# Kernel optimization log

Hardware: AMD Instinct MI355X
Metric: run time of the kernel (lower is better)

## Reference

```python
import jax, jax.numpy as jnp
import numpy as np

M = 64; N_SC = 32; SPS = 8; LENCP = 16; NUMOFDM = 256 // N_SC
BETA = 0.5; SPAN = 16; LENRRC = SPAN * SPS + 1  # 129
FC = 25e6; FS = 10e6 * SPS
CLIP = 1.2; SNR = 10.0; THRES = 8.0
LEN_T = NUMOFDM * (M + LENCP)              # 640
NUMSAMPLES = LEN_T * SPS + LENRRC * 2      # 5378
L1 = LEN_T * SPS + LENRRC - 1              # 5248 (post pulse-shaping length)


def make_rrc():
    # standard root-raised-cosine, unit energy
    t = np.arange(-SPAN * SPS // 2, SPAN * SPS // 2 + 1) / SPS
    h = np.zeros_like(t)
    eps = 1e-9
    t0 = np.abs(t) < eps
    ts = np.abs(np.abs(t) - 1.0 / (4 * BETA)) < eps
    reg = ~(t0 | ts)
    tr = t[reg]
    h[reg] = (np.sin(np.pi * tr * (1 - BETA)) + 4 * BETA * tr * np.cos(np.pi * tr * (1 + BETA))) / (
        np.pi * tr * (1 - (4 * BETA * tr) ** 2))
    h[t0] = 1 + BETA * (4 / np.pi - 1)
    h[ts] = (BETA / np.sqrt(2)) * ((1 + 2 / np.pi) * np.sin(np.pi / (4 * BETA)) +
                                   (1 - 2 / np.pi) * np.cos(np.pi / (4 * BETA)))
    h = h / np.sqrt(np.sum(h ** 2))
    return h.astype(np.float32)


def _conv_full(u, k):
    # torch F.conv1d(x, k.flip(), padding=K-1) == full convolution with k
    K = k.shape[0]
    return jax.lax.conv_general_dilated(
        u[:, None, :], k[::-1][None, None, :], (1,), [(K - 1, K - 1)],
        dimension_numbers=('NCH', 'OIH', 'NCH'))[:, 0, :]


def _pulse_filter(c, rrc):
    return _conv_full(c.real, rrc) + 1j * _conv_full(c.imag, rrc)


def _power_norm(z):
    m = jnp.mean(z, axis=1, keepdims=True)
    s = jnp.std(z, axis=1, ddof=1, keepdims=True)  # torch.std is unbiased
    return (z - m) / (s + 1e-8)


def _forward(x, W_enc, b_enc, W_dec, b_dec, rrc, awgn, startloc):
    B = x.shape[0]
    # --- encoder (linear proxy for ResNetTx) -> 512 reals ---
    z = x.reshape(B, -1) @ W_enc + b_enc
    z = _power_norm(z)
    c = z.reshape(B, 256, 2)
    c = (c[..., 0] + 1j * c[..., 1]).reshape(B, NUMOFDM, N_SC)  # complex64
    # --- DFT precoding ---
    c = jnp.fft.fftshift(jnp.fft.fft(c, axis=-1, norm='ortho'), axes=-1)
    # --- subcarrier mapping (contiguous block, mapping==1) ---
    loc = jnp.arange(startloc, startloc + N_SC)
    data_f = jnp.zeros((B, NUMOFDM, M), jnp.complex64).at[:, :, loc].set(c)
    data_t = jnp.fft.ifft(data_f, axis=-1, norm='ortho')
    data_t = jnp.concatenate([data_t[:, :, -LENCP:], data_t], axis=-1)  # CP
    data_t = data_t.reshape(B, LEN_T)
    # --- zero-stuffed upsampling + RRC pulse shaping ---
    over = jnp.zeros((B, LEN_T * SPS), jnp.complex64).at[:, ::SPS].set(data_t)
    xc = _pulse_filter(over, rrc)  # (B, L1)
    # --- carrier mixing ---
    n = jnp.arange(NUMSAMPLES, dtype=jnp.float32)
    cos_c = jnp.sqrt(2.0) * jnp.cos(2 * jnp.pi * FC * n / FS)
    sin_c = jnp.sqrt(2.0) * jnp.sin(2 * jnp.pi * FC * n / FS)
    data_x = xc.real * cos_c[:L1] - xc.imag * sin_c[:L1]
    # --- clipping ---
    thr = CLIP * jnp.sqrt(jnp.mean(jnp.square(data_x), axis=1, keepdims=True))
    over_amp = jax.nn.relu(jnp.abs(data_x) - thr)
    data_x = (1.0 - over_amp / (jnp.abs(data_x) + 1e-8)) * data_x
    # --- PAPR ---
    tstart = (LENRRC + 1) // 2
    p = jnp.square(data_x[:, tstart:tstart + LEN_T * SPS])
    PAPRdB = 10.0 * jnp.log10(jnp.max(p, axis=1) / jnp.mean(p, axis=1))
    PAPRloss = jnp.mean(jax.nn.relu(PAPRdB - THRES))
    # --- AWGN channel (no fading) ---
    data_r = data_x + awgn
    # --- downconversion + matched filter ---
    rc = data_r * cos_c[:L1] - 1j * (data_r * sin_c[:L1])
    filt = _pulse_filter(rc, rrc)  # (B, L1 + LENRRC - 1) = (B, 5376)
    y = filt[:, LENRRC - 1:filt.shape[1] - LENRRC:SPS]  # (B, LEN_T)
    y = y.reshape(B, NUMOFDM, M + LENCP)[:, :, LENCP:]
    y = jnp.fft.fft(y, axis=-1, norm='ortho')[:, :, loc]
    y = jnp.fft.ifft(jnp.fft.fftshift(y, axes=-1), axis=-1, norm='ortho')
    y = y.reshape(B, NUMOFDM * N_SC)
    y = jnp.stack([y.real, y.imag], axis=-1).reshape(B, 8, 8, 8)
    # --- decoder (linear proxy for ResNetRx) ---
    out = (y.reshape(B, 512) @ W_dec + b_dec).reshape(B, 3, 32, 32)
    return out, PAPRdB, PAPRloss


def setup_inputs() -> dict:
    key = jax.random.key(0)
    ks = jax.random.split(key, 4)
    B = 1024
    x = jax.random.normal(ks[0], (B, 3, 32, 32), jnp.float32)
    W_enc = jax.random.normal(ks[1], (3072, 512), jnp.float32) * 0.02
    b_enc = jnp.zeros((512,), jnp.float32)
    W_dec = jax.random.normal(ks[2], (512, 3072), jnp.float32) * 0.05
    b_dec = jnp.zeros((3072,), jnp.float32)
    rrc = jnp.asarray(make_rrc())
    noise_std = 10.0 ** (-SNR / 20.0)
    awgn = jax.random.normal(ks[3], (B, L1), jnp.float32) * noise_std
    return {"x": x, "W_enc": W_enc, "b_enc": b_enc, "W_dec": W_dec,
            "b_dec": b_dec, "rrc": rrc, "awgn": awgn, "startloc": 7}


def reference(x, W_enc, b_enc, W_dec, b_dec, rrc, awgn, startloc):
    return _forward(x, W_enc, b_enc, W_dec, b_dec, rrc, awgn, startloc)
```

## Files before the change

### kernel.cpp

```cpp
#include <hip/hip_runtime.h>
#include <hip/hip_bf16.h>
#include <math.h>

#define L1_     5248
#define LENRRC_ 129
#define TSTART_ 65
#define NWIN_   5120
#define SWZ(m) ((m) + ((m) >> 3))

typedef __attribute__((ext_vector_type(8))) short s16x8;
typedef __attribute__((ext_vector_type(4))) float f32x4;

__device__ inline ushort bf16_rne(float x) {
    unsigned xb = __float_as_uint(x);
    return (ushort)((xb + 0x7fffu + ((xb >> 16) & 1u)) >> 16);
}

__device__ inline float wave_sum(float v) {
    #pragma unroll
    for (int m = 32; m > 0; m >>= 1) v += __shfl_xor(v, m, 64);
    return v;
}
__device__ inline float wave_max(float v) {
    #pragma unroll
    for (int m = 32; m > 0; m >>= 1) v = fmaxf(v, __shfl_xor(v, m, 64));
    return v;
}

__global__ __launch_bounds__(256) void pack_k(const float* __restrict__ x,
        const float* __restrict__ W1, const float* __restrict__ W2,
        const float* __restrict__ benc,
        ushort* __restrict__ xb, ushort* __restrict__ w1t, ushort* __restrict__ w2t,
        float* __restrict__ z)
{
    __shared__ ushort tile[64][70];
    const int blk = blockIdx.x, tid = threadIdx.x;
    if (blk < 3072) {
        int i = blk * 256 + tid;
        float4 v = ((const float4*)x)[i];
        ushort4 h;
        h.x = bf16_rne(v.x); h.y = bf16_rne(v.y);
        h.z = bf16_rne(v.z); h.w = bf16_rne(v.w);
        ((ushort4*)xb)[i] = h;
    } else if (blk < 3840) {
        const float* W; ushort* T; int K, N, n0, k0;
        if (blk < 3456) {
            int idx = blk - 3072;
            W = W1; T = w1t; K = 3072; N = 512;
            n0 = (idx & 7) * 64; k0 = (idx >> 3) * 64;
        } else {
            int idx = blk - 3456;
            W = W2; T = w2t; K = 512; N = 3072;
            n0 = (idx % 48) * 64; k0 = (idx / 48) * 64;
        }
        const int cr = tid >> 4, cc = (tid & 15) * 4;
        #pragma unroll
        for (int i = 0; i < 4; ++i) {
            int kk = i * 16 + cr;
            float4 v = *(const float4*)&W[(size_t)(k0 + kk) * N + n0 + cc];
            tile[kk][cc]     = bf16_rne(v.x);
            tile[kk][cc + 1] = bf16_rne(v.y);
            tile[kk][cc + 2] = bf16_rne(v.z);
            tile[kk][cc + 3] = bf16_rne(v.w);
        }
        __syncthreads();
        #pragma unroll
        for (int i = 0; i < 4; ++i) {
            int nn = i * 16 + cr;
            ushort4 h;
            h.x = tile[cc][nn]; h.y = tile[cc + 1][nn];
            h.z = tile[cc + 2][nn]; h.w = tile[cc + 3][nn];
            *(ushort4*)&T[(size_t)(n0 + nn) * K + k0 + cc] = h;
        }
    } else {
        int i = (blk - 3840) * 256 + tid;
        z[i] = benc[i & 511];
    }
}

__global__ __launch_bounds__(256) void gemm1_k(const ushort* __restrict__ Ab,
        const ushort* __restrict__ Bb, float* __restrict__ C, int M, int N, int K,
        int partial)
{
    __shared__ ushort Asl[64 * 72];
    __shared__ ushort Bsl[128 * 72];
    const int tid = threadIdx.x;
    const int lane = tid & 63, wave = tid >> 6;
    const int wm = (wave >> 1) * 32, wn = (wave & 1) * 64;
    const int m0 = blockIdx.y * 64, n0 = blockIdx.x * 128;
    const int kch = K / 8, kbeg = blockIdx.z * kch, kend = kbeg + kch;
    const int fm = lane & 15, q = lane >> 4;
    f32x4 acc[2][4] = {};

    for (int kt = kbeg; kt < kend; kt += 64) {
        #pragma unroll
        for (int i = 0; i < 2; ++i) {
            int c = i * 256 + tid;
            int row = c >> 3, k8 = (c & 7) * 8;
            *(uint4*)&Asl[row * 72 + k8] =
                *(const uint4*)&Ab[(size_t)(m0 + row) * K + kt + k8];
        }
        #pragma unroll
        for (int i = 0; i < 4; ++i) {
            int c = i * 256 + tid;
            int row = c >> 3, k8 = (c & 7) * 8;
            *(uint4*)&Bsl[row * 72 + k8] =
                *(const uint4*)&Bb[(size_t)(n0 + row) * K + kt + k8];
        }
        __syncthreads();
        #pragma unroll
        for (int ks = 0; ks < 2; ++ks) {
            s16x8 a[2], b[4];
            #pragma unroll
            for (int mf = 0; mf < 2; ++mf)
                a[mf] = *(const s16x8*)&Asl[(wm + mf * 16 + fm) * 72 + ks * 32 + q * 8];
            #pragma unroll
            for (int nf = 0; nf < 4; ++nf)
                b[nf] = *(const s16x8*)&Bsl[(wn + nf * 16 + fm) * 72 + ks * 32 + q * 8];
            #pragma unroll
            for (int mf = 0; mf < 2; ++mf)
                #pragma unroll
                for (int nf = 0; nf < 4; ++nf)
                    acc[mf][nf] = __builtin_amdgcn_mfma_f32_16x16x32_bf16(a[mf], b[nf], acc[mf][nf], 0, 0, 0);
        }
        __syncthreads();
    }

    if (partial) {
        float* Cs = C + (size_t)blockIdx.z * ((size_t)M * N);
        #pragma unroll
        for (int mf = 0; mf < 2; ++mf)
            #pragma unroll
            for (int nf = 0; nf < 4; ++nf)
                #pragma unroll
                for (int r = 0; r < 4; ++r) {
                    int m = m0 + wm + mf * 16 + q * 4 + r;
                    int n = n0 + wn + nf * 16 + fm;
                    Cs[(size_t)m * N + n] = acc[mf][nf][r];
                }
    } else {
        #pragma unroll
        for (int mf = 0; mf < 2; ++mf)
            #pragma unroll
            for (int nf = 0; nf < 4; ++nf)
                #pragma unroll
                for (int r = 0; r < 4; ++r) {
                    int m = m0 + wm + mf * 16 + q * 4 + r;
                    int n = n0 + wn + nf * 16 + fm;
                    atomicAdd(&C[(size_t)m * N + n], acc[mf][nf][r]);
                }
    }
}

__global__ __launch_bounds__(256) void gemm2_k(const ushort* __restrict__ Ab,
        const ushort* __restrict__ Bb, const float* __restrict__ bias,
        const float* __restrict__ papr, float* __restrict__ C,
        float* __restrict__ out_loss, int M, int N, int K)
{
    __shared__ ushort Asl[64 * 72];
    __shared__ ushort Bsl[64 * 72];
    __shared__ float red[4];
    const int tid = threadIdx.x;
    const int lane = tid & 63, wave = tid >> 6;
    const int wm = (wave >> 1) * 32, wn = (wave & 1) * 32;
    const int m0 = blockIdx.y * 64, n0 = blockIdx.x * 64;
    const int fm = lane & 15, q = lane >> 4;
    f32x4 acc[2][2] = {};

    for (int kt = 0; kt < K; kt += 64) {
        #pragma unroll
        for (int i = 0; i < 2; ++i) {
            int c = i * 256 + tid;
            int row = c >> 3, k8 = (c & 7) * 8;
            *(uint4*)&Asl[row * 72 + k8] =
                *(const uint4*)&Ab[(size_t)(m0 + row) * K + kt + k8];
            *(uint4*)&Bsl[row * 72 + k8] =
                *(const uint4*)&Bb[(size_t)(n0 + row) * K + kt + k8];
        }
        __syncthreads();
        #pragma unroll
        for (int ks = 0; ks < 2; ++ks) {
            s16x8 a[2], b[2];
            #pragma unroll
            for (int mf = 0; mf < 2; ++mf)
                a[mf] = *(const s16x8*)&Asl[(wm + mf * 16 + fm) * 72 + ks * 32 + q * 8];
            #pragma unroll
            for (int nf = 0; nf < 2; ++nf)
                b[nf] = *(const s16x8*)&Bsl[(wn + nf * 16 + fm) * 72 + ks * 32 + q * 8];
            #pragma unroll
            for (int mf = 0; mf < 2; ++mf)
                #pragma unroll
                for (int nf = 0; nf < 2; ++nf)
                    acc[mf][nf] = __builtin_amdgcn_mfma_f32_16x16x32_bf16(a[mf], b[nf], acc[mf][nf], 0, 0, 0);
        }
        __syncthreads();
    }

    #pragma unroll
    for (int mf = 0; mf < 2; ++mf)
        #pragma unroll
        for (int nf = 0; nf < 2; ++nf)
            #pragma unroll
            for (int r = 0; r < 4; ++r) {
                int m = m0 + wm + mf * 16 + q * 4 + r;
                int n = n0 + wn + nf * 16 + fm;
                C[(size_t)m * N + n] = acc[mf][nf][r] + bias[n];
            }

    if (blockIdx.x == 0 && blockIdx.y == 0) {
        float s = 0.f;
        for (int i = tid; i < 1024; i += 256) { float v = papr[i] - 8.f; s += v > 0.f ? v : 0.f; }
        s = wave_sum(s);
        if (lane == 0) red[wave] = s;
        __syncthreads();
        if (tid == 0) *out_loss = (red[0] + red[1] + red[2] + red[3]) * (1.f / 1024.f);
    }
}

__global__ __launch_bounds__(256) void mega_k(const float* __restrict__ z,
        const float* __restrict__ benc,
        const float* __restrict__ rrc, const float* __restrict__ awgn,
        const int* __restrict__ slocp, ushort* __restrict__ y5b,
        float* __restrict__ papr, float* __restrict__ out_papr, int nsp)
{
    __shared__ float  zl[512];
    __shared__ float2 frfi[8][32];
    __shared__ float2 trti[672];
    __shared__ float  hl[132];
    __shared__ float  csl[16], ssl[16];
    __shared__ float2 cs64[64];
    __shared__ float2 gcs[130];
    __shared__ float  dxr[SWZ(L1_ - 1) + 1];
    __shared__ float2 wrli[512];
    __shared__ float  red[4], red2[4];

    const int b = blockIdx.x, tid = threadIdx.x;
    const int lane = tid & 63, wv = tid >> 6;
    const int sloc = *slocp;

    if (tid < 64) {
        float ang = 0.09817477042468103f * (float)tid;
        float s, c; sincosf(ang, &s, &c);
        cs64[tid] = make_float2(c, s);
    }
    if (tid >= 64 && tid < 80) {
        int t = tid - 64;
        float ang = 1.9634954084936207f * (float)t;
        float s, c; sincosf(ang, &s, &c);
        csl[t] = 1.4142135623730951f * c; ssl[t] = 1.4142135623730951f * s;
    }
    if (tid >= 96 && tid < 128) {
        int t = tid - 96;
        int idx = (t < 16) ? t : (640 + t);
        trti[idx] = make_float2(0.f, 0.f);
    }
    for (int e = tid; e < LENRRC_; e += 256) hl[e] = rrc[e];

    float v0, v1;
    if (nsp) {
        v0 = benc[tid]; v1 = benc[tid + 256];
        const float* zp = z + (size_t)b * 512;
        #pragma unroll
        for (int s = 0; s < 8; ++s) {
            v0 += zp[(size_t)s * 524288 + tid];
            v1 += zp[(size_t)s * 524288 + tid + 256];
        }
    } else {
        v0 = z[(size_t)b * 512 + tid];
        v1 = z[(size_t)b * 512 + tid + 256];
    }
    __syncthreads();

    if (tid < LENRRC_) {
        int neg = (16 - (tid & 15)) & 15;
        gcs[tid] = make_float2(hl[tid] * csl[neg], hl[tid] * ssl[neg]);
    }

    {
        float S = wave_sum(v0 + v1);
        float Q = wave_sum(v0 * v0 + v1 * v1);
        if (lane == 0) { red[wv] = S; red2[wv] = Q; }
    }
    __syncthreads();
    {
        float S = red[0] + red[1] + red[2] + red[3];
        float Q = red2[0] + red2[1] + red2[2] + red2[3];
        float mean = S * (1.f / 512.f);
        float var = (Q - S * mean) * (1.f / 511.f);
        float inv = 1.f / (sqrtf(var) + 1e-8f);
        zl[tid] = (v0 - mean) * inv; zl[tid + 256] = (v1 - mean) * inv;
    }
    __syncthreads();

    {
        int s = tid >> 5, kk = tid & 31;
        int kk2 = (kk + 16) & 31;
        float sr = 0.f, si = 0.f;
        int t2 = 0;
        for (int q = 0; q < 32; ++q) {
            float2 w = cs64[2 * t2];
            float2 c = *(const float2*)&zl[(s * 32 + q) * 2];
            sr += c.x * w.x + c.y * w.y;
            si += c.y * w.x - c.x * w.y;
            t2 = (t2 + kk2) & 31;
        }
        frfi[s][kk] = make_float2(sr * 0.1767766952966369f, si * 0.1767766952966369f);
    }
    __syncthreads();

    {
        int s = tid >> 5, n = tid & 31;
        float er = 0.f, ei = 0.f, or_ = 0.f, oi = 0.f;
        int t = (sloc * n) & 63;
        for (int k = 0; k < 32; k += 2) {
            float2 w = cs64[t];
            float2 f = frfi[s][k];
            er += f.x * w.x - f.y * w.y;
            ei += f.y * w.x + f.x * w.y;
            t = (t + n) & 63;
            w = cs64[t];
            f = frfi[s][k + 1];
            or_ += f.x * w.x - f.y * w.y;
            oi  += f.y * w.x + f.x * w.y;
            t = (t + n) & 63;
        }
        float sgn = (sloc & 1) ? -1.f : 1.f;
        float dr0 = (er + or_) * 0.125f, di0 = (ei + oi) * 0.125f;
        float dr1 = sgn * (er - or_) * 0.125f, di1 = sgn * (ei - oi) * 0.125f;
        int base = s * 80;
        trti[base + 32 + n] = make_float2(dr0, di0);
        trti[base + 64 + n] = make_float2(dr1, di1);
        if (n >= 16) trti[base + n] = make_float2(dr1, di1);
    }
    __syncthreads();

    float ss = 0.f;
    for (int a = tid; a < 656; a += 256) {
        float accr[8] = {}, acci[8] = {};
        #pragma unroll 4
        for (int d = 0; d < 16; ++d) {
            float2 tv = trti[16 + a - d];
            #pragma unroll
            for (int r = 0; r < 8; ++r) {
                float h = hl[r + 8 * d];
                accr[r] += tv.x * h; acci[r] += tv.y * h;
            }
        }
        {
            float2 tv = trti[a];
            float h = hl[128];
            accr[0] += tv.x * h; acci[0] += tv.y * h;
        }
        int cb = (a & 1) * 8;
        #pragma unroll
        for (int r = 0; r < 8; ++r) {
            float v = accr[r] * csl[cb + r] - acci[r] * ssl[cb + r];
            dxr[SWZ(a * 8 + r)] = v;
            ss += v * v;
        }
    }
    ss = wave_sum(ss);
    if (lane == 0) red[wv] = ss;
    __syncthreads();
    float thr = 1.2f * sqrtf((red[0] + red[1] + red[2] + red[3]) / (float)L1_);
    __syncthreads();

    float pmax = 0.f, psum = 0.f;
    for (int i = tid; i < L1_; i += 256) {
        float x = dxr[SWZ(i)];
        float ax = fabsf(x);
        float over = ax - thr; over = over > 0.f ? over : 0.f;
        float y = (1.f - over / (ax + 1e-8f)) * x;
        if (i >= TSTART_ && i < TSTART_ + NWIN_) { float p = y * y; psum += p; pmax = fmaxf(pmax, p); }
        dxr[SWZ(i)] = y + awgn[(size_t)b * L1_ + i];
    }
    psum = wave_sum(psum); pmax = wave_max(pmax);
    if (lane == 0) { red[wv] = psum; red2[wv] = pmax; }
    __syncthreads();
    if (tid == 0) {
        float sum = red[0] + red[1] + red[2] + red[3];
        float mx = fmaxf(fmaxf(red2[0], red2[1]), fmaxf(red2[2], red2[3]));
        float pdb = 10.f * log10f(mx / (sum / (float)NWIN_));
        papr[b] = pdb;
        out_papr[b] = pdb;
    }
    __syncthreads();

    #pragma unroll
    for (int j0 = 0; j0 < 2; ++j0) {
        int j = j0 * 256 + tid;
        int s = j >> 6, n = j & 63;
        int T = s * 80 + n + 32;
        int base = 9 * T;
        int db = 0;
        float ar = 0.f, ai = 0.f;
        for (int e = 0; e < 16; ++e) {
            #pragma unroll
            for (int u = 0; u < 8; ++u) {
                int off = (u == 0) ? 0 : (u + 1);
                float v = dxr[base - off];
                float2 g = gcs[db + u];
                ar += v * g.x; ai += v * g.y;
            }
            base -= 9; db += 8;
        }
        { float v = dxr[base]; float2 g = gcs[128]; ar += v * g.x; ai += v * g.y; }
        float sr = (n & 1) ? -ar : ar;
        float si = (n & 1) ? ai : -ai;
        wrli[j] = make_float2(sr, si);
    }
    __syncthreads();

    {
        int s = tid >> 5, n = tid & 31;
        float2 d0 = wrli[s * 64 + n];
        float2 d1 = wrli[s * 64 + n + 32];
        trti[s * 32 + n]       = make_float2(d0.x + d1.x, d0.y + d1.y);
        trti[256 + s * 32 + n] = make_float2(d0.x - d1.x, d0.y - d1.y);
    }
    __syncthreads();

    {
        int s = tid >> 5, kk = tid & 31;
        int f = sloc + kk;
        const float2* dsel = &trti[((f & 1) ? 256 : 0) + s * 32];
        float vr = 0.f, vi = 0.f;
        int t = 0;
        for (int n = 0; n < 32; ++n) {
            float2 w = cs64[t];
            float2 d = dsel[n];
            vr += d.x * w.x + d.y * w.y;
            vi += d.y * w.x - d.x * w.y;
            t = (t + f) & 63;
        }
        int ksh = (kk + 16) & 31;
        frfi[s][ksh] = make_float2(vr * 0.125f, vi * 0.125f);
    }
    __syncthreads();

    {
        int s = tid >> 5, q2 = tid & 31;
        float ur = 0.f, ui = 0.f;
        int t2 = 0;
        for (int k = 0; k < 32; ++k) {
            float2 w = cs64[2 * t2];
            float2 f = frfi[s][k];
            ur += f.x * w.x - f.y * w.y;
            ui += f.y * w.x + f.x * w.y;
            t2 = (t2 + q2) & 31;
        }
        ur *= 0.1767766952966369f; ui *= 0.1767766952966369f;
        ushort2 hv; hv.x = bf16_rne(ur); hv.y = bf16_rne(ui);
        *(ushort2*)&y5b[(size_t)b * 512 + (s * 32 + q2) * 2] = hv;
    }
}

extern "C" void kernel_launch(void* const* d_in, const int* in_sizes, int n_in,
                              void* d_out, int out_size, void* d_ws, size_t ws_size,
                              hipStream_t stream) {
    const float* x    = (const float*)d_in[0];
    const float* Wenc = (const float*)d_in[1];
    const float* benc = (const float*)d_in[2];
    const float* Wdec = (const float*)d_in[3];
    const float* bdec = (const float*)d_in[4];
    const float* rrc  = (const float*)d_in[5];
    const float* awgn = (const float*)d_in[6];
    const int* sloc   = (const int*)d_in[7];
    float* out = (float*)d_out;

    char* wsb = (char*)d_ws;
    ushort* xb   = (ushort*)wsb;                     wsb += (size_t)1024 * 3072 * 2;
    ushort* w1t  = (ushort*)wsb;                     wsb += (size_t)512 * 3072 * 2;
    ushort* w2t  = (ushort*)wsb;                     wsb += (size_t)3072 * 512 * 2;
    ushort* y5b  = (ushort*)wsb;                     wsb += (size_t)1024 * 512 * 2;
    float*  papr = (float*)wsb;                      wsb += 1024 * 4;
    float*  zbuf = (float*)wsb;
    size_t head = (size_t)((char*)zbuf - (char*)d_ws);
    int partial = (ws_size >= head + (size_t)8 * 1024 * 512 * 4) ? 1 : 0;

    float* out_papr = out + (size_t)1024 * 3072;
    float* out_loss = out_papr + 1024;

    pack_k<<<partial ? 3840 : 5888, 256, 0, stream>>>(x, Wenc, Wdec, benc, xb, w1t, w2t, zbuf);
    gemm1_k<<<dim3(4, 16, 8), 256, 0, stream>>>(xb, w1t, zbuf, 1024, 512, 3072, partial);
    mega_k<<<1024, 256, 0, stream>>>(zbuf, benc, rrc, awgn, sloc, y5b, papr, out_papr,
                                     partial ? 8 : 0);
    gemm2_k<<<dim3(48, 16, 1), 256, 0, stream>>>(y5b, w2t, bdec, papr, out, out_loss, 1024, 3072, 512);
}
```

Baseline: 173.8 us.

## Use direct global-to-LDS loads with XOR swizzle in GEMMs and tune mega kernel loops

Both GEMM kernels now stage A/B tiles with global_load_lds (direct global-to-LDS DMA) instead of register round-trips. They replace the padded 72-stride layout with an unpadded 64-stride layout that uses an XOR swizzle to avoid bank conflicts. The mega kernel gets an occupancy hint, unroll pragmas on its small DFT loops, float4-vectorised awgn loads in the clipping pass, and a fused two-output receive filter loop that shares coefficient loads. This mixes several unrelated micro-optimisations, and the swizzled LDS addressing must line up exactly with the DMA destination layout.

Measured after the change: 147.2 us. 15.3% less time.

```diff
diff --git a/kernel.cpp b/kernel.cpp
--- a/kernel.cpp
+++ b/kernel.cpp
@@ -25,6 +25,12 @@
     #pragma unroll
     for (int m = 32; m > 0; m >>= 1) v = fmaxf(v, __shfl_xor(v, m, 64));
     return v;
+}
+
+__device__ inline void gl_lds16(const void* g, void* l) {
+    __builtin_amdgcn_global_load_lds(
+        (const __attribute__((address_space(1))) unsigned int*)g,
+        (__attribute__((address_space(3))) unsigned int*)l, 16, 0, 0);
 }
 
 __global__ __launch_bounds__(256) void pack_k(const float* __restrict__ x,
@@ -82,8 +88,8 @@
         const ushort* __restrict__ Bb, float* __restrict__ C, int M, int N, int K,
         int partial)
 {
-    __shared__ ushort Asl[64 * 72];
-    __shared__ ushort Bsl[128 * 72];
+    __shared__ __attribute__((aligned(16))) ushort Asl[64 * 64];
+    __shared__ __attribute__((aligned(16))) ushort Bsl[128 * 64];
     const int tid = threadIdx.x;
     const int lane = tid & 63, wave = tid >> 6;
     const int wm = (wave >> 1) * 32, wn = (wave & 1) * 64;
@@ -92,31 +98,41 @@
     const int fm = lane & 15, q = lane >> 4;
     f32x4 acc[2][4] = {};
 
+    int arow[2], akb[2], brow[4], bkb[4];
+    #pragma unroll
+    for (int j = 0; j < 2; ++j) {
+        int c = ((wave * 2 + j) << 6) + lane;
+        arow[j] = c >> 3; akb[j] = (c & 7) ^ (arow[j] & 7);
+    }
+    #pragma unroll
+    for (int j = 0; j < 4; ++j) {
+        int c = ((wave * 4 + j) << 6) + lane;
+        brow[j] = c >> 3; bkb[j] = (c & 7) ^ (brow[j] & 7);
+    }
+
     for (int kt = kbeg; kt < kend; kt += 64) {
         #pragma unroll
-        for (int i = 0; i < 2; ++i) {
-            int c = i * 256 + tid;
-            int row = c >> 3, k8 = (c & 7) * 8;
-            *(uint4*)&Asl[row * 72 + k8] =
-                *(const uint4*)&Ab[(size_t)(m0 + row) * K + kt + k8];
-        }
-        #pragma unroll
-        for (int i = 0; i < 4; ++i) {
-            int c = i * 256 + tid;
-            int row = c >> 3, k8 = (c & 7) * 8;
-            *(uint4*)&Bsl[row * 72 + k8] =
-                *(const uint4*)&Bb[(size_t)(n0 + row) * K + kt + k8];
-        }
+        for (int j = 0; j < 2; ++j)
+            gl_lds16(&Ab[(size_t)(m0 + arow[j]) * K + kt + akb[j] * 8],
+                     &Asl[(wave * 2 + j) << 9]);
+        #pragma unroll
+        for (int j = 0; j < 4; ++j)
+            gl_lds16(&Bb[(size_t)(n0 + brow[j]) * K + kt + bkb[j] * 8],
+                     &Bsl[(wave * 4 + j) << 9]);
         __syncthreads();
         #pragma unroll
         for (int ks = 0; ks < 2; ++ks) {
             s16x8 a[2], b[4];
             #pragma unroll
-            for (int mf = 0; mf < 2; ++mf)
-                a[mf] = *(const s16x8*)&Asl[(wm + mf * 16 + fm) * 72 + ks * 32 + q * 8];
-            #pragma unroll
-            for (int nf = 0; nf < 4; ++nf)
-                b[nf] = *(const s16x8*)&Bsl[(wn + nf * 16 + fm) * 72 + ks * 32 + q * 8];
+            for (int mf = 0; mf < 2; ++mf) {
+                int r = wm + mf * 16 + fm;
+                a[mf] = *(const s16x8*)&Asl[(r << 6) + ((((ks << 2) + q) ^ (r & 7)) << 3)];
+            }
+            #pragma unroll
+            for (int nf = 0; nf < 4; ++nf) {
+                int r = wn + nf * 16 + fm;
+                b[nf] = *(const s16x8*)&Bsl[(r << 6) + ((((ks << 2) + q) ^ (r & 7)) << 3)];
+            }
             #pragma unroll
             for (int mf = 0; mf < 2; ++mf)
                 #pragma unroll
@@ -157,8 +173,8 @@
         const float* __restrict__ papr, float* __restrict__ C,
         float* __restrict__ out_loss, int M, int N, int K)
 {
-    __shared__ ushort Asl[64 * 72];
-    __shared__ ushort Bsl[64 * 72];
+    __shared__ __attribute__((aligned(16))) ushort Asl[64 * 64];
+    __shared__ __attribute__((aligned(16))) ushort Bsl[64 * 64];
     __shared__ float red[4];
     const int tid = threadIdx.x;
     const int lane = tid & 63, wave = tid >> 6;
@@ -167,26 +183,35 @@
     const int fm = lane & 15, q = lane >> 4;
     f32x4 acc[2][2] = {};
 
+    int srow[2], skb[2];
+    #pragma unroll
+    for (int j = 0; j < 2; ++j) {
+        int c = ((wave * 2 + j) << 6) + lane;
+        srow[j] = c >> 3; skb[j] = (c & 7) ^ (srow[j] & 7);
+    }
+
     for (int kt = 0; kt < K; kt += 64) {
         #pragma unroll
-        for (int i = 0; i < 2; ++i) {
-            int c = i * 256 + tid;
-            int row = c >> 3, k8 = (c & 7) * 8;
-            *(uint4*)&Asl[row * 72 + k8] =
-                *(const uint4*)&Ab[(size_t)(m0 + row) * K + kt + k8];
-            *(uint4*)&Bsl[row * 72 + k8] =
-                *(const uint4*)&Bb[(size_t)(n0 + row) * K + kt + k8];
+        for (int j = 0; j < 2; ++j) {
+            gl_lds16(&Ab[(size_t)(m0 + srow[j]) * K + kt + skb[j] * 8],
+                     &Asl[(wave * 2 + j) << 9]);
+            gl_lds16(&Bb[(size_t)(n0 + srow[j]) * K + kt + skb[j] * 8],
+                     &Bsl[(wave * 2 + j) << 9]);
         }
         __syncthreads();
         #pragma unroll
         for (int ks = 0; ks < 2; ++ks) {
             s16x8 a[2], b[2];
             #pragma unroll
-            for (int mf = 0; mf < 2; ++mf)
-                a[mf] = *(const s16x8*)&Asl[(wm + mf * 16 + fm) * 72 + ks * 32 + q * 8];
-            #pragma unroll
-            for (int nf = 0; nf < 2; ++nf)
-                b[nf] = *(const s16x8*)&Bsl[(wn + nf * 16 + fm) * 72 + ks * 32 + q * 8];
+            for (int mf = 0; mf < 2; ++mf) {
+                int r = wm + mf * 16 + fm;
+                a[mf] = *(const s16x8*)&Asl[(r << 6) + ((((ks << 2) + q) ^ (r & 7)) << 3)];
+            }
+            #pragma unroll
+            for (int nf = 0; nf < 2; ++nf) {
+                int r = wn + nf * 16 + fm;
+                b[nf] = *(const s16x8*)&Bsl[(r << 6) + ((((ks << 2) + q) ^ (r & 7)) << 3)];
+            }
             #pragma unroll
             for (int mf = 0; mf < 2; ++mf)
                 #pragma unroll
@@ -217,7 +242,7 @@
     }
 }
 
-__global__ __launch_bounds__(256) void mega_k(const float* __restrict__ z,
+__global__ __launch_bounds__(256, 4) void mega_k(const float* __restrict__ z,
         const float* __restrict__ benc,
         const float* __restrict__ rrc, const float* __restrict__ awgn,
         const int* __restrict__ slocp, ushort* __restrict__ y5b,
@@ -297,6 +322,7 @@
         int kk2 = (kk + 16) & 31;
         float sr = 0.f, si = 0.f;
         int t2 = 0;
+        #pragma unroll 4
         for (int q = 0; q < 32; ++q) {
             float2 w = cs64[2 * t2];
             float2 c = *(const float2*)&zl[(s * 32 + q) * 2];
@@ -312,6 +338,7 @@
         int s = tid >> 5, n = tid & 31;
         float er = 0.f, ei = 0.f, or_ = 0.f, oi = 0.f;
         int t = (sloc * n) & 63;
+        #pragma unroll 2
         for (int k = 0; k < 32; k += 2) {
             float2 w = cs64[t];
             float2 f = frfi[s][k];
@@ -366,13 +393,25 @@
     __syncthreads();
 
     float pmax = 0.f, psum = 0.f;
-    for (int i = tid; i < L1_; i += 256) {
-        float x = dxr[SWZ(i)];
-        float ax = fabsf(x);
-        float over = ax - thr; over = over > 0.f ? over : 0.f;
-        float y = (1.f - over / (ax + 1e-8f)) * x;
-        if (i >= TSTART_ && i < TSTART_ + NWIN_) { float p = y * y; psum += p; pmax = fmaxf(pmax, p); }
-        dxr[SWZ(i)] = y + awgn[(size_t)b * L1_ + i];
+    {
+        const float4* ag = (const float4*)&awgn[(size_t)b * L1_];
+        for (int ii = tid; ii < 1312; ii += 256) {
+            float4 aw = ag[ii];
+            int i = ii * 4;
+            #pragma unroll
+            for (int e = 0; e < 4; ++e) {
+                int idx = i + e;
+                float x = dxr[SWZ(idx)];
+                float ax = fabsf(x);
+                float over = fmaxf(ax - thr, 0.f);
+                float y = (1.f - over / (ax + 1e-8f)) * x;
+                if (idx >= TSTART_ && idx < TSTART_ + NWIN_) {
+                    float p = y * y; psum += p; pmax = fmaxf(pmax, p);
+                }
+                float awv = (e == 0) ? aw.x : (e == 1) ? aw.y : (e == 2) ? aw.z : aw.w;
+                dxr[SWZ(idx)] = y + awv;
+            }
+        }
     }
     psum = wave_sum(psum); pmax = wave_max(pmax);
     if (lane == 0) { red[wv] = psum; red2[wv] = pmax; }
@@ -386,28 +425,35 @@
     }
     __syncthreads();
 
-    #pragma unroll
-    for (int j0 = 0; j0 < 2; ++j0) {
-        int j = j0 * 256 + tid;
-        int s = j >> 6, n = j & 63;
-        int T = s * 80 + n + 32;
-        int base = 9 * T;
+    {
+        int s = tid >> 6, n = tid & 63;
+        int T0 = s * 80 + n + 32;
+        int base0 = 9 * T0;
+        int base1 = 9 * (T0 + 320);
+        float ar0 = 0.f, ai0 = 0.f, ar1 = 0.f, ai1 = 0.f;
         int db = 0;
-        float ar = 0.f, ai = 0.f;
+        #pragma unroll 2
         for (int e = 0; e < 16; ++e) {
             #pragma unroll
             for (int u = 0; u < 8; ++u) {
                 int off = (u == 0) ? 0 : (u + 1);
-                float v = dxr[base - off];
                 float2 g = gcs[db + u];
-                ar += v * g.x; ai += v * g.y;
-            }
-            base -= 9; db += 8;
-        }
-        { float v = dxr[base]; float2 g = gcs[128]; ar += v * g.x; ai += v * g.y; }
-        float sr = (n & 1) ? -ar : ar;
-        float si = (n & 1) ? ai : -ai;
-        wrli[j] = make_float2(sr, si);
+                float va = dxr[base0 - off];
+                float vb = dxr[base1 - off];
+                ar0 += va * g.x; ai0 += va * g.y;
+                ar1 += vb * g.x; ai1 += vb * g.y;
+            }
+            base0 -= 9; base1 -= 9; db += 8;
+        }
+        {
+            float2 g = gcs[128];
+            float va = dxr[base0], vb = dxr[base1];
+            ar0 += va * g.x; ai0 += va * g.y;
+            ar1 += vb * g.x; ai1 += vb * g.y;
+        }
+        bool odd = (n & 1);
+        wrli[tid]       = make_float2(odd ? -ar0 : ar0, odd ? ai0 : -ai0);
+        wrli[tid + 256] = make_float2(odd ? -ar1 : ar1, odd ? ai1 : -ai1);
     }
     __syncthreads();
 
@@ -426,6 +472,7 @@
         const float2* dsel = &trti[((f & 1) ? 256 : 0) + s * 32];
         float vr = 0.f, vi = 0.f;
         int t = 0;
+        #pragma unroll 4
         for (int n = 0; n < 32; ++n) {
             float2 w = cs64[t];
             float2 d = dsel[n];
@@ -442,6 +489,7 @@
         int s = tid >> 5, q2 = tid & 31;
         float ur = 0.f, ui = 0.f;
         int t2 = 0;
+        #pragma unroll 4
         for (int k = 0; k < 32; ++k) {
             float2 w = cs64[2 * t2];
             float2 f = frfi[s][k];
```
